# Kernel tuning notes

Hardware: AMD Instinct MI355X
Metric: run time of the kernel (lower is better)

## Reference

```python
import jax, jax.numpy as jnp
import numpy as np

OFFSET_SCALE = 6.0  # self.offset_scale in the torch module
HW = 256
N_PTS = HW * HW  # 65536


def _kpt2tform(kpt_src, kpt_dst):
    # kpt_src, kpt_dst: [K,3]. Scaled Kabsch/Procrustes (torch kpt2Tform).
    # norm of (row0 - row0) is exactly 0, so summing rows 1: is identical math
    # (and avoids a 0-norm which is non-differentiable in the bwd version).
    sum_dist1 = jnp.sum(jnp.linalg.norm(kpt_src[1:] - kpt_src[0], axis=1))
    sum_dist2 = jnp.sum(jnp.linalg.norm(kpt_dst[1:] - kpt_dst[0], axis=1))
    s = sum_dist2 / sum_dist1
    A = kpt_src * s
    Bm = kpt_dst
    AA = A - A.mean(axis=0)
    BB = Bm - Bm.mean(axis=0)
    H = AA.T @ BB  # [3,3]
    U, S, Vh = jnp.linalg.svd(H, full_matrices=False)
    V = Vh.T  # torch.svd returns V s.t. H = U S V^T; jnp returns Vh
    R = V @ U.T
    t = jnp.mean(Bm - A @ R.T, axis=0)
    return R * s, t


def reference(Offset, Posmap_kpt, mean_posmap, uv_kpt):
    B = Offset.shape[0]
    # offsetmap: [B,256,256,3]
    offsetmap = jnp.transpose(Offset * OFFSET_SCALE + mean_posmap[None], (0, 2, 3, 1))
    kptmap = jnp.transpose(Posmap_kpt, (0, 2, 3, 1))
    kpt_dst = kptmap[:, uv_kpt[:, 0], uv_kpt[:, 1]]    # [B,68,3]
    kpt_src = offsetmap[:, uv_kpt[:, 0], uv_kpt[:, 1]]  # [B,68,3]
    pts = offsetmap.reshape(B, N_PTS, 3)
    R, t = jax.vmap(_kpt2tform)(kpt_src, kpt_dst)  # R:[B,3,3], t:[B,3]
    # outpos[i] = pts[i] @ R[i].T + t[i]
    outpos = jnp.einsum('bnc,brc->bnr', pts, R) + t[:, None, :]
    return jnp.transpose(outpos.reshape(B, HW, HW, 3), (0, 3, 1, 2))


def setup_inputs():
    key = jax.random.key(0)
    k1, k2, k3, k4 = jax.random.split(key, 4)
    B = 128
    return {
        "Offset": jax.random.normal(k1, (B, 3, HW, HW), dtype=jnp.float32),
        "Posmap_kpt": jax.random.normal(k2, (B, 3, HW, HW), dtype=jnp.float32),
        "mean_posmap": jax.random.normal(k3, (3, HW, HW), dtype=jnp.float32),
        "uv_kpt": jax.random.randint(k4, (68, 2), 0, HW, dtype=jnp.int32),
    }
```

## Files before the change

### kernel.cpp

```cpp
#include <hip/hip_runtime.h>
#include <math.h>

#define HW 256
#define NPTS (HW * HW)
#define NP4 (NPTS / 4)
#define NKPT 68
#define NBATCH 128
#define KB 4

typedef float f32x4 __attribute__((ext_vector_type(4)));

__global__ __launch_bounds__(128) void kpt_tform_kernel(
    const float* __restrict__ Offset,
    const float* __restrict__ Posmap,
    const float* __restrict__ meanp,
    const int*   __restrict__ uv,
    float* __restrict__ Rt)
{
    const int b    = blockIdx.x;
    const int i    = threadIdx.x;
    const int wave = i >> 6;
    const int lane = i & 63;

    __shared__ float s0[6];
    __shared__ float partial[2][17];

    float src[3] = {0.f, 0.f, 0.f};
    float dst[3] = {0.f, 0.f, 0.f};

    if (i < NKPT) {
        const int u = uv[2 * i + 0];
        const int v = uv[2 * i + 1];
        const int pix = u * HW + v;
        const float* ob = Offset + (size_t)b * 3 * NPTS;
        const float* pb = Posmap + (size_t)b * 3 * NPTS;
#pragma unroll
        for (int c = 0; c < 3; ++c) {
            src[c] = fmaf(ob[c * NPTS + pix], 6.0f, meanp[c * NPTS + pix]);
            dst[c] = pb[c * NPTS + pix];
        }
    }
    if (i == 0) {
#pragma unroll
        for (int c = 0; c < 3; ++c) { s0[c] = src[c]; s0[3 + c] = dst[c]; }
    }
    __syncthreads();

    float vals[17];
    float d1 = 0.f, d2 = 0.f;
    if (i >= 1 && i < NKPT) {
        float dx = src[0] - s0[0], dy = src[1] - s0[1], dz = src[2] - s0[2];
        d1 = sqrtf(dx * dx + dy * dy + dz * dz);
        dx = dst[0] - s0[3]; dy = dst[1] - s0[4]; dz = dst[2] - s0[5];
        d2 = sqrtf(dx * dx + dy * dy + dz * dz);
    }
    vals[0] = d1;
    vals[1] = d2;
#pragma unroll
    for (int c = 0; c < 3; ++c) { vals[2 + c] = src[c]; vals[5 + c] = dst[c]; }
#pragma unroll
    for (int r = 0; r < 3; ++r)
#pragma unroll
        for (int c = 0; c < 3; ++c)
            vals[8 + r * 3 + c] = src[r] * dst[c];

#pragma unroll
    for (int j = 0; j < 17; ++j) {
        float v = vals[j];
#pragma unroll
        for (int off = 32; off > 0; off >>= 1)
            v += __shfl_down(v, off);
        if (lane == 0) partial[wave][j] = v;
    }
    __syncthreads();
    if (i != 0) return;

    float sum[17];
#pragma unroll
    for (int j = 0; j < 17; ++j) sum[j] = partial[0][j] + partial[1][j];

    const float s = sum[1] / sum[0];
    const float invN = 1.0f / (float)NKPT;
    float mS[3], mD[3];
#pragma unroll
    for (int c = 0; c < 3; ++c) { mS[c] = sum[2 + c] * invN; mD[c] = sum[5 + c] * invN; }

    float Hm[3][3];
#pragma unroll
    for (int r = 0; r < 3; ++r)
#pragma unroll
        for (int c = 0; c < 3; ++c)
            Hm[r][c] = sum[8 + r * 3 + c] - (float)NKPT * mS[r] * mD[c];

    float X[3][3];
#pragma unroll
    for (int r = 0; r < 3; ++r)
#pragma unroll
        for (int c = 0; c < 3; ++c)
            X[r][c] = Hm[c][r];

    float nf = 0.f;
#pragma unroll
    for (int r = 0; r < 3; ++r)
#pragma unroll
        for (int c = 0; c < 3; ++c)
            nf += X[r][c] * X[r][c];
    nf = rsqrtf(nf);
#pragma unroll
    for (int r = 0; r < 3; ++r)
#pragma unroll
        for (int c = 0; c < 3; ++c)
            X[r][c] *= nf;

    for (int it = 0; it < 18; ++it) {
        float C[3][3];
        C[0][0] = X[1][1] * X[2][2] - X[1][2] * X[2][1];
        C[0][1] = X[1][2] * X[2][0] - X[1][0] * X[2][2];
        C[0][2] = X[1][0] * X[2][1] - X[1][1] * X[2][0];
        C[1][0] = X[2][1] * X[0][2] - X[2][2] * X[0][1];
        C[1][1] = X[2][2] * X[0][0] - X[2][0] * X[0][2];
        C[1][2] = X[2][0] * X[0][1] - X[2][1] * X[0][0];
        C[2][0] = X[0][1] * X[1][2] - X[0][2] * X[1][1];
        C[2][1] = X[0][2] * X[1][0] - X[0][0] * X[1][2];
        C[2][2] = X[0][0] * X[1][1] - X[0][1] * X[1][0];
        const float det = X[0][0] * C[0][0] + X[0][1] * C[0][1] + X[0][2] * C[0][2];
        const float inv = 0.5f / det;
#pragma unroll
        for (int r = 0; r < 3; ++r)
#pragma unroll
            for (int c = 0; c < 3; ++c)
                X[r][c] = 0.5f * X[r][c] + C[r][c] * inv;
    }

    float* o = Rt + b * 12;
#pragma unroll
    for (int r = 0; r < 3; ++r) {
#pragma unroll
        for (int c = 0; c < 3; ++c)
            o[r * 3 + c] = s * X[r][c];
        o[9 + r] = mD[r] - s * (X[r][0] * mS[0] + X[r][1] * mS[1] + X[r][2] * mS[2]);
    }
}

__global__ __launch_bounds__(256) void apply_tform_kernel(
    const f32x4* __restrict__ Off,
    const f32x4* __restrict__ meanp,
    const float* __restrict__ Rt,
    f32x4* __restrict__ out)
{
    const int b0 = blockIdx.y * KB;
    const int g  = blockIdx.x * blockDim.x + threadIdx.x;

    __shared__ float srt[12 * KB];
    if (threadIdx.x < 12 * KB) srt[threadIdx.x] = Rt[b0 * 12 + threadIdx.x];
    __syncthreads();

    const f32x4 mx = meanp[0 * NP4 + g];
    const f32x4 my = meanp[1 * NP4 + g];
    const f32x4 mz = meanp[2 * NP4 + g];

#pragma unroll
    for (int k = 0; k < KB; ++k) {
        const float* R = &srt[12 * k];
        const float R00 = R[0], R01 = R[1], R02 = R[2];
        const float R10 = R[3], R11 = R[4], R12 = R[5];
        const float R20 = R[6], R21 = R[7], R22 = R[8];
        const float t0 = R[9], t1 = R[10], t2 = R[11];

        const size_t base = (size_t)(b0 + k) * 3 * NP4;
        const f32x4 ox = Off[base + 0 * NP4 + g];
        const f32x4 oy = Off[base + 1 * NP4 + g];
        const f32x4 oz = Off[base + 2 * NP4 + g];

        f32x4 r0, r1, r2;
#pragma unroll
        for (int j = 0; j < 4; ++j) {
            const float px = fmaf(ox[j], 6.0f, mx[j]);
            const float py = fmaf(oy[j], 6.0f, my[j]);
            const float pz = fmaf(oz[j], 6.0f, mz[j]);
            r0[j] = fmaf(R00, px, fmaf(R01, py, fmaf(R02, pz, t0)));
            r1[j] = fmaf(R10, px, fmaf(R11, py, fmaf(R12, pz, t1)));
            r2[j] = fmaf(R20, px, fmaf(R21, py, fmaf(R22, pz, t2)));
        }

        out[base + 0 * NP4 + g] = r0;
        out[base + 1 * NP4 + g] = r1;
        out[base + 2 * NP4 + g] = r2;
    }
}

extern "C" void kernel_launch(void* const* d_in, const int* in_sizes, int n_in,
                              void* d_out, int out_size, void* d_ws, size_t ws_size,
                              hipStream_t stream) {
    const float* Offset = (const float*)d_in[0];
    const float* Posmap = (const float*)d_in[1];
    const float* meanp  = (const float*)d_in[2];
    const int*   uv     = (const int*)d_in[3];
    float* out = (float*)d_out;
    float* Rt  = (float*)d_ws;

    kpt_tform_kernel<<<NBATCH, 128, 0, stream>>>(Offset, Posmap, meanp, uv, Rt);

    dim3 grid(NP4 / 256, NBATCH / KB);
    apply_tform_kernel<<<grid, 256, 0, stream>>>(
        (const f32x4*)Offset, (const f32x4*)meanp, Rt, (f32x4*)out);
}
```

Baseline: 44.20 us.

## Fuse keypoint transform solve into apply kernel, recomputing per block

Merges the two launches into one kernel. Each of the four waves in a block solves the scaled Procrustes transform for one batch, with two keypoints per lane, and the block then applies those transforms to its pixel tile. This removes a kernel launch and the workspace round trip, but every block along the pixel axis redundantly recomputes the gathers and the polar iteration (64x redundancy). The iteration count also drops from 18 to 16, which may slightly affect accuracy.

```diff
diff --git a/kernel.cpp b/kernel.cpp
--- a/kernel.cpp
+++ b/kernel.cpp
@@ -10,154 +10,153 @@
 
 typedef float f32x4 __attribute__((ext_vector_type(4)));
 
-__global__ __launch_bounds__(128) void kpt_tform_kernel(
+__global__ __launch_bounds__(256) void fused_rebuild_kernel(
     const float* __restrict__ Offset,
     const float* __restrict__ Posmap,
     const float* __restrict__ meanp,
     const int*   __restrict__ uv,
-    float* __restrict__ Rt)
+    const f32x4* __restrict__ Off4,
+    const f32x4* __restrict__ mean4,
+    f32x4* __restrict__ out)
 {
-    const int b    = blockIdx.x;
-    const int i    = threadIdx.x;
-    const int wave = i >> 6;
-    const int lane = i & 63;
-
-    __shared__ float s0[6];
-    __shared__ float partial[2][17];
-
-    float src[3] = {0.f, 0.f, 0.f};
-    float dst[3] = {0.f, 0.f, 0.f};
-
-    if (i < NKPT) {
-        const int u = uv[2 * i + 0];
-        const int v = uv[2 * i + 1];
-        const int pix = u * HW + v;
+    const int tid  = threadIdx.x;
+    const int wv   = tid >> 6;
+    const int lane = tid & 63;
+    const int b0   = blockIdx.y * KB;
+
+    __shared__ float srt[12 * KB];
+
+    {
+        const int b = b0 + wv;
         const float* ob = Offset + (size_t)b * 3 * NPTS;
         const float* pb = Posmap + (size_t)b * 3 * NPTS;
+
+        float sA[3], dA[3], sB[3] = {0.f, 0.f, 0.f}, dB[3] = {0.f, 0.f, 0.f};
+        {
+            const int pix = uv[2 * lane] * HW + uv[2 * lane + 1];
+#pragma unroll
+            for (int c = 0; c < 3; ++c) {
+                sA[c] = fmaf(ob[c * NPTS + pix], 6.0f, meanp[c * NPTS + pix]);
+                dA[c] = pb[c * NPTS + pix];
+            }
+        }
+        const bool has2 = lane < (NKPT - 64);
+        if (has2) {
+            const int kp = 64 + lane;
+            const int pix = uv[2 * kp] * HW + uv[2 * kp + 1];
+#pragma unroll
+            for (int c = 0; c < 3; ++c) {
+                sB[c] = fmaf(ob[c * NPTS + pix], 6.0f, meanp[c * NPTS + pix]);
+                dB[c] = pb[c * NPTS + pix];
+            }
+        }
+
+        const float s0x = __shfl(sA[0], 0), s0y = __shfl(sA[1], 0), s0z = __shfl(sA[2], 0);
+        const float d0x = __shfl(dA[0], 0), d0y = __shfl(dA[1], 0), d0z = __shfl(dA[2], 0);
+
+        float vals[17];
+        float dd1 = 0.f, dd2 = 0.f;
+        if (lane > 0) {
+            float dx = sA[0] - s0x, dy = sA[1] - s0y, dz = sA[2] - s0z;
+            dd1 = sqrtf(dx * dx + dy * dy + dz * dz);
+            dx = dA[0] - d0x; dy = dA[1] - d0y; dz = dA[2] - d0z;
+            dd2 = sqrtf(dx * dx + dy * dy + dz * dz);
+        }
+        if (has2) {
+            float dx = sB[0] - s0x, dy = sB[1] - s0y, dz = sB[2] - s0z;
+            dd1 += sqrtf(dx * dx + dy * dy + dz * dz);
+            dx = dB[0] - d0x; dy = dB[1] - d0y; dz = dB[2] - d0z;
+            dd2 += sqrtf(dx * dx + dy * dy + dz * dz);
+        }
+        vals[0] = dd1;
+        vals[1] = dd2;
 #pragma unroll
         for (int c = 0; c < 3; ++c) {
-            src[c] = fmaf(ob[c * NPTS + pix], 6.0f, meanp[c * NPTS + pix]);
-            dst[c] = pb[c * NPTS + pix];
-        }
-    }
-    if (i == 0) {
-#pragma unroll
-        for (int c = 0; c < 3; ++c) { s0[c] = src[c]; s0[3 + c] = dst[c]; }
+            vals[2 + c] = sA[c] + sB[c];
+            vals[5 + c] = dA[c] + dB[c];
+        }
+#pragma unroll
+        for (int r = 0; r < 3; ++r)
+#pragma unroll
+            for (int c = 0; c < 3; ++c)
+                vals[8 + r * 3 + c] = sA[r] * dA[c] + sB[r] * dB[c];
+
+#pragma unroll
+        for (int j = 0; j < 17; ++j) {
+            float v = vals[j];
+#pragma unroll
+            for (int off = 32; off > 0; off >>= 1)
+                v += __shfl_down(v, off);
+            vals[j] = v;
+        }
+
+        if (lane == 0) {
+            const float s = vals[1] / vals[0];
+            const float invN = 1.0f / (float)NKPT;
+            float mS[3], mD[3];
+#pragma unroll
+            for (int c = 0; c < 3; ++c) {
+                mS[c] = vals[2 + c] * invN;
+                mD[c] = vals[5 + c] * invN;
+            }
+
+            float X[3][3];
+#pragma unroll
+            for (int r = 0; r < 3; ++r)
+#pragma unroll
+                for (int c = 0; c < 3; ++c)
+                    X[c][r] = vals[8 + r * 3 + c] - (float)NKPT * mS[r] * mD[c];
+
+            float nf = 0.f;
+#pragma unroll
+            for (int r = 0; r < 3; ++r)
+#pragma unroll
+                for (int c = 0; c < 3; ++c)
+                    nf += X[r][c] * X[r][c];
+            nf = rsqrtf(nf);
+#pragma unroll
+            for (int r = 0; r < 3; ++r)
+#pragma unroll
+                for (int c = 0; c < 3; ++c)
+                    X[r][c] *= nf;
+
+            for (int it = 0; it < 16; ++it) {
+                float C[3][3];
+                C[0][0] = X[1][1] * X[2][2] - X[1][2] * X[2][1];
+                C[0][1] = X[1][2] * X[2][0] - X[1][0] * X[2][2];
+                C[0][2] = X[1][0] * X[2][1] - X[1][1] * X[2][0];
+                C[1][0] = X[2][1] * X[0][2] - X[2][2] * X[0][1];
+                C[1][1] = X[2][2] * X[0][0] - X[2][0] * X[0][2];
+                C[1][2] = X[2][0] * X[0][1] - X[2][1] * X[0][0];
+                C[2][0] = X[0][1] * X[1][2] - X[0][2] * X[1][1];
+                C[2][1] = X[0][2] * X[1][0] - X[0][0] * X[1][2];
+                C[2][2] = X[0][0] * X[1][1] - X[0][1] * X[1][0];
+                const float det = X[0][0] * C[0][0] + X[0][1] * C[0][1] + X[0][2] * C[0][2];
+                const float inv = 0.5f / det;
+#pragma unroll
+                for (int r = 0; r < 3; ++r)
+#pragma unroll
+                    for (int c = 0; c < 3; ++c)
+                        X[r][c] = 0.5f * X[r][c] + C[r][c] * inv;
+            }
+
+            float* o = &srt[12 * wv];
+#pragma unroll
+            for (int r = 0; r < 3; ++r) {
+#pragma unroll
+                for (int c = 0; c < 3; ++c)
+                    o[r * 3 + c] = s * X[r][c];
+                o[9 + r] = mD[r] - s * (X[r][0] * mS[0] + X[r][1] * mS[1] + X[r][2] * mS[2]);
+            }
+        }
     }
     __syncthreads();
 
-    float vals[17];
-    float d1 = 0.f, d2 = 0.f;
-    if (i >= 1 && i < NKPT) {
-        float dx = src[0] - s0[0], dy = src[1] - s0[1], dz = src[2] - s0[2];
-        d1 = sqrtf(dx * dx + dy * dy + dz * dz);
-        dx = dst[0] - s0[3]; dy = dst[1] - s0[4]; dz = dst[2] - s0[5];
-        d2 = sqrtf(dx * dx + dy * dy + dz * dz);
-    }
-    vals[0] = d1;
-    vals[1] = d2;
-#pragma unroll
-    for (int c = 0; c < 3; ++c) { vals[2 + c] = src[c]; vals[5 + c] = dst[c]; }
-#pragma unroll
-    for (int r = 0; r < 3; ++r)
-#pragma unroll
-        for (int c = 0; c < 3; ++c)
-            vals[8 + r * 3 + c] = src[r] * dst[c];
-
-#pragma unroll
-    for (int j = 0; j < 17; ++j) {
-        float v = vals[j];
-#pragma unroll
-        for (int off = 32; off > 0; off >>= 1)
-            v += __shfl_down(v, off);
-        if (lane == 0) partial[wave][j] = v;
-    }
-    __syncthreads();
-    if (i != 0) return;
-
-    float sum[17];
-#pragma unroll
-    for (int j = 0; j < 17; ++j) sum[j] = partial[0][j] + partial[1][j];
-
-    const float s = sum[1] / sum[0];
-    const float invN = 1.0f / (float)NKPT;
-    float mS[3], mD[3];
-#pragma unroll
-    for (int c = 0; c < 3; ++c) { mS[c] = sum[2 + c] * invN; mD[c] = sum[5 + c] * invN; }
-
-    float Hm[3][3];
-#pragma unroll
-    for (int r = 0; r < 3; ++r)
-#pragma unroll
-        for (int c = 0; c < 3; ++c)
-            Hm[r][c] = sum[8 + r * 3 + c] - (float)NKPT * mS[r] * mD[c];
-
-    float X[3][3];
-#pragma unroll
-    for (int r = 0; r < 3; ++r)
-#pragma unroll
-        for (int c = 0; c < 3; ++c)
-            X[r][c] = Hm[c][r];
-
-    float nf = 0.f;
-#pragma unroll
-    for (int r = 0; r < 3; ++r)
-#pragma unroll
-        for (int c = 0; c < 3; ++c)
-            nf += X[r][c] * X[r][c];
-    nf = rsqrtf(nf);
-#pragma unroll
-    for (int r = 0; r < 3; ++r)
-#pragma unroll
-        for (int c = 0; c < 3; ++c)
-            X[r][c] *= nf;
-
-    for (int it = 0; it < 18; ++it) {
-        float C[3][3];
-        C[0][0] = X[1][1] * X[2][2] - X[1][2] * X[2][1];
-        C[0][1] = X[1][2] * X[2][0] - X[1][0] * X[2][2];
-        C[0][2] = X[1][0] * X[2][1] - X[1][1] * X[2][0];
-        C[1][0] = X[2][1] * X[0][2] - X[2][2] * X[0][1];
-        C[1][1] = X[2][2] * X[0][0] - X[2][0] * X[0][2];
-        C[1][2] = X[2][0] * X[0][1] - X[2][1] * X[0][0];
-        C[2][0] = X[0][1] * X[1][2] - X[0][2] * X[1][1];
-        C[2][1] = X[0][2] * X[1][0] - X[0][0] * X[1][2];
-        C[2][2] = X[0][0] * X[1][1] - X[0][1] * X[1][0];
-        const float det = X[0][0] * C[0][0] + X[0][1] * C[0][1] + X[0][2] * C[0][2];
-        const float inv = 0.5f / det;
-#pragma unroll
-        for (int r = 0; r < 3; ++r)
-#pragma unroll
-            for (int c = 0; c < 3; ++c)
-                X[r][c] = 0.5f * X[r][c] + C[r][c] * inv;
-    }
-
-    float* o = Rt + b * 12;
-#pragma unroll
-    for (int r = 0; r < 3; ++r) {
-#pragma unroll
-        for (int c = 0; c < 3; ++c)
-            o[r * 3 + c] = s * X[r][c];
-        o[9 + r] = mD[r] - s * (X[r][0] * mS[0] + X[r][1] * mS[1] + X[r][2] * mS[2]);
-    }
-}
-
-__global__ __launch_bounds__(256) void apply_tform_kernel(
-    const f32x4* __restrict__ Off,
-    const f32x4* __restrict__ meanp,
-    const float* __restrict__ Rt,
-    f32x4* __restrict__ out)
-{
-    const int b0 = blockIdx.y * KB;
-    const int g  = blockIdx.x * blockDim.x + threadIdx.x;
-
-    __shared__ float srt[12 * KB];
-    if (threadIdx.x < 12 * KB) srt[threadIdx.x] = Rt[b0 * 12 + threadIdx.x];
-    __syncthreads();
-
-    const f32x4 mx = meanp[0 * NP4 + g];
-    const f32x4 my = meanp[1 * NP4 + g];
-    const f32x4 mz = meanp[2 * NP4 + g];
+    const int g = blockIdx.x * blockDim.x + tid;
+
+    const f32x4 mx = mean4[0 * NP4 + g];
+    const f32x4 my = mean4[1 * NP4 + g];
+    const f32x4 mz = mean4[2 * NP4 + g];
 
 #pragma unroll
     for (int k = 0; k < KB; ++k) {
@@ -168,9 +167,9 @@
         const float t0 = R[9], t1 = R[10], t2 = R[11];
 
         const size_t base = (size_t)(b0 + k) * 3 * NP4;
-        const f32x4 ox = Off[base + 0 * NP4 + g];
-        const f32x4 oy = Off[base + 1 * NP4 + g];
-        const f32x4 oz = Off[base + 2 * NP4 + g];
+        const f32x4 ox = Off4[base + 0 * NP4 + g];
+        const f32x4 oy = Off4[base + 1 * NP4 + g];
+        const f32x4 oz = Off4[base + 2 * NP4 + g];
 
         f32x4 r0, r1, r2;
 #pragma unroll
@@ -197,11 +196,9 @@
     const float* meanp  = (const float*)d_in[2];
     const int*   uv     = (const int*)d_in[3];
     float* out = (float*)d_out;
-    float* Rt  = (float*)d_ws;
-
-    kpt_tform_kernel<<<NBATCH, 128, 0, stream>>>(Offset, Posmap, meanp, uv, Rt);
 
     dim3 grid(NP4 / 256, NBATCH / KB);
-    apply_tform_kernel<<<grid, 256, 0, stream>>>(
-        (const f32x4*)Offset, (const f32x4*)meanp, Rt, (f32x4*)out);
+    fused_rebuild_kernel<<<grid, 256, 0, stream>>>(
+        Offset, Posmap, meanp, uv,
+        (const f32x4*)Offset, (const f32x4*)meanp, (f32x4*)out);
 }
```

Result: slower. 48.82 us (+10.5%).
